# Kernel tuning notes

Measured on AMD Instinct MI355X. Metric: run time of the kernel, lower is better.

Reference implementation:

```python
import jax, jax.numpy as jnp
import numpy as np
from jax import lax

DIM = 1152
HEADS = 16
HEAD_DIM = 72  # HEADS*HEAD_DIM == DIM
HID = 4608     # int(DIM*4.0)
B = 2
N = 4096
EPS_RMS = 1e-6
EPS_LA = 1e-15


def setup_inputs() -> dict:
    key = jax.random.key(0)
    ks = jax.random.split(key, 12)
    w = lambda k, shape: (jax.random.normal(k, shape, jnp.float32) * 0.02)
    z = lambda n: jnp.zeros((n,), jnp.float32)
    return {
        "hidden_states": jax.random.normal(ks[0], (B, N, DIM), jnp.float32),
        "temb": jax.random.normal(ks[1], (B, 6 * DIM), jnp.float32),
        "scale_shift_table": jax.random.normal(ks[2], (6, DIM), jnp.float32) / np.float32(np.sqrt(DIM)),
        "Wq": w(ks[3], (DIM, DIM)), "bq": z(DIM),
        "Wk": w(ks[4], (DIM, DIM)), "bk": z(DIM),
        "Wv": w(ks[5], (DIM, DIM)), "bv": z(DIM),
        "Wo": w(ks[6], (DIM, DIM)), "bo": z(DIM),
        "W_inv": w(ks[7], (2 * HID, DIM)), "b_inv": z(2 * HID),   # 1x1 conv dim -> 2*hid
        "W_dw": w(ks[8], (2 * HID, 3)), "b_dw": z(2 * HID),       # depthwise k=3
        "W_pt": w(ks[9], (DIM, HID)),                              # 1x1 conv hid -> dim, no bias
    }


def _rms(x):
    # RMSNorm, elementwise_affine=False, eps=1e-6
    return x * lax.rsqrt(jnp.mean(x * x, axis=-1, keepdims=True) + EPS_RMS)


def reference(hidden_states, temb, scale_shift_table, Wq, bq, Wk, bk, Wv, bv, Wo, bo,
              W_inv, b_inv, W_dw, b_dw, W_pt):
    Bn, Nn, D = hidden_states.shape
    # adaLN-single modulation
    mods = scale_shift_table[None] + temb.reshape(Bn, 6, D)  # (B,6,D)
    shift_msa, scale_msa, gate_msa, shift_mlp, scale_mlp, gate_mlp = (
        mods[:, i][:, None, :] for i in range(6))  # each (B,1,D)

    x = _rms(hidden_states) * (1.0 + scale_msa) + shift_msa

    # --- Lite linear attention (ReLU kernel, denominator via padded-ones value) ---
    q = jax.nn.relu(x @ Wq.T + bq).reshape(Bn, Nn, HEADS, HEAD_DIM).transpose(0, 2, 1, 3)  # bhnd
    k = jax.nn.relu(x @ Wk.T + bk).reshape(Bn, Nn, HEADS, HEAD_DIM).transpose(0, 2, 1, 3)
    v = (x @ Wv.T + bv).reshape(Bn, Nn, HEADS, HEAD_DIM).transpose(0, 2, 1, 3)
    v = jnp.pad(v, ((0, 0), (0, 0), (0, 0), (0, 1)), constant_values=1.0)  # (B,h,N,d+1)
    kv = jnp.einsum('bhnd,bhne->bhde', k, v)        # (B,h,d,d+1)
    out = jnp.einsum('bhnd,bhde->bhne', q, kv)      # (B,h,N,d+1)
    out = out[..., :-1] / (out[..., -1:] + EPS_LA)  # numerator / denominator
    out = out.transpose(0, 2, 1, 3).reshape(Bn, Nn, D)
    attn_out = out @ Wo.T + bo

    hidden_states = gate_msa * attn_out + hidden_states

    # --- GLUMBConv FFN ---
    y = _rms(hidden_states) * (1.0 + scale_mlp) + shift_mlp
    y = jax.nn.silu(y @ W_inv.T + b_inv)            # inverted 1x1 conv + SiLU, (B,N,2*HID)
    yc = y.transpose(0, 2, 1)                        # (B,2*HID,N)
    yc = lax.conv_general_dilated(
        yc, W_dw[:, None, :], window_strides=(1,), padding=[(1, 1)],
        feature_group_count=2 * HID,
        dimension_numbers=('NCH', 'OIH', 'NCH')) + b_dw[None, :, None]
    xg, gate = jnp.split(yc, 2, axis=1)
    y = (xg * jax.nn.silu(gate)).transpose(0, 2, 1)  # (B,N,HID)
    ff = y @ W_pt.T                                   # point conv, no bias

    return hidden_states + gate_mlp * ff
```

## Files before the change

kernel.cpp:

```cpp
#include <hip/hip_runtime.h>
#include <hip/hip_bf16.h>

typedef __hip_bfloat16 bf16;
typedef short short8 __attribute__((ext_vector_type(8)));
typedef short short4v __attribute__((ext_vector_type(4)));
typedef float floatx4 __attribute__((ext_vector_type(4)));
typedef int int4v __attribute__((ext_vector_type(4)));

#define DIMC 1152
#define NTOK 8192
#define NSEQ 4096
#define HD 72
#define HDP 73
#define HIDC 4608
#define HID2 9216
#define QKVN 3456
#define KVH (HD * HDP)
#define PZ ((size_t)2048 * DIMC)
#define PZB ((size_t)4096 * DIMC)

#define DP 96
#define KVNT 128
#define KV_NITER 2
#define KV_CHUNKS 16

__device__ __forceinline__ float b2f(bf16 x) { return __bfloat162float(x); }
__device__ __forceinline__ bf16 f2b(float x) { return __float2bfloat16(x); }
__device__ __forceinline__ void st(float* p, float v) { *p = v; }
__device__ __forceinline__ void st(bf16* p, float v)  { *p = f2b(v); }
__device__ __forceinline__ float tf(float x) { return x; }
__device__ __forceinline__ float tf(bf16 x)  { return __bfloat162float(x); }
__device__ __forceinline__ float s2f(short s) {
    unsigned int u = ((unsigned int)(unsigned short)s) << 16;
    return __uint_as_float(u);
}
__device__ __forceinline__ short f2s(float f) {
    bf16 h = f2b(f);
    return *reinterpret_cast<short*>(&h);
}

__device__ __forceinline__ void gload_lds16(const bf16* g, short* l) {
    __builtin_amdgcn_global_load_lds(
        (const __attribute__((address_space(1))) void*)g,
        (__attribute__((address_space(3))) void*)l, 16, 0, 0);
}

__global__ void cvt_all_kernel(const float* __restrict__ s0, const float* __restrict__ s1,
                               const float* __restrict__ s2, const float* __restrict__ s3,
                               const float* __restrict__ s4, const float* __restrict__ s5,
                               bf16* __restrict__ dst) {
    int i = blockIdx.x * 256 + threadIdx.x;
    if (i >= 5308416) return;
    const float* src; int base;
    if (i < 1327104) {
        if (i < 331776)      { src = s0; base = 0; }
        else if (i < 663552) { src = s1; base = 331776; }
        else if (i < 995328) { src = s2; base = 663552; }
        else                 { src = s3; base = 995328; }
    } else if (i < 3981312)  { src = s4; base = 1327104; }
    else                     { src = s5; base = 3981312; }
    floatx4 v = ((const floatx4*)src)[i - base];
    bf16* o = dst + (size_t)i * 4;
    o[0] = f2b(v[0]); o[1] = f2b(v[1]); o[2] = f2b(v[2]); o[3] = f2b(v[3]);
}

__global__ void prep_kernel(const float* __restrict__ sst, const float* __restrict__ temb,
                            float* __restrict__ mods, const float* __restrict__ ba,
                            const float* __restrict__ bb, const float* __restrict__ bc,
                            float* __restrict__ bq) {
    int i = blockIdx.x * 256 + threadIdx.x;
    if (i < 2 * 6 * DIMC) {
        mods[i] = sst[i % (6 * DIMC)] + temb[i];
    } else if (i < 2 * 6 * DIMC + DIMC) {
        int j = i - 2 * 6 * DIMC;
        bq[j] = ba[j]; bq[j + DIMC] = bb[j]; bq[j + 2 * DIMC] = bc[j];
    }
}

template<typename T>
__global__ void rmsmod_kernel(const T* __restrict__ h, const float* __restrict__ mods,
                              int shift_idx, int scale_idx, bf16* __restrict__ xout) {
    int token = blockIdx.x;
    int b = token >> 12;
    int tid = threadIdx.x;
    int wave = tid >> 6, lane = tid & 63;
    const T* hp = h + (size_t)token * DIMC;

    float v[8];
    float s = 0.f;
    if (tid < 144) {
        if constexpr (sizeof(T) == 4) {
            floatx4 a = *(const floatx4*)((const float*)hp + tid * 8);
            floatx4 c = *(const floatx4*)((const float*)hp + tid * 8 + 4);
            v[0]=a[0]; v[1]=a[1]; v[2]=a[2]; v[3]=a[3];
            v[4]=c[0]; v[5]=c[1]; v[6]=c[2]; v[7]=c[3];
        } else {
            short8 a = *(const short8*)((const short*)hp + tid * 8);
            #pragma unroll
            for (int j = 0; j < 8; j++) v[j] = s2f(a[j]);
        }
        #pragma unroll
        for (int j = 0; j < 8; j++) s += v[j] * v[j];
    }
    #pragma unroll
    for (int off = 32; off > 0; off >>= 1) s += __shfl_down(s, off);
    __shared__ float wsum[4];
    if (lane == 0) wsum[wave] = s;
    __syncthreads();
    float tot = wsum[0] + wsum[1] + wsum[2] + wsum[3];
    float r = rsqrtf(tot / (float)DIMC + 1e-6f);

    if (tid < 144) {
        const float* sh = mods + (size_t)(b * 6 + shift_idx) * DIMC + tid * 8;
        const float* sc = mods + (size_t)(b * 6 + scale_idx) * DIMC + tid * 8;
        floatx4 sh0 = *(const floatx4*)sh, sh1 = *(const floatx4*)(sh + 4);
        floatx4 sc0 = *(const floatx4*)sc, sc1 = *(const floatx4*)(sc + 4);
        short8 o;
        o[0] = f2s(v[0] * r * (1.f + sc0[0]) + sh0[0]);
        o[1] = f2s(v[1] * r * (1.f + sc0[1]) + sh0[1]);
        o[2] = f2s(v[2] * r * (1.f + sc0[2]) + sh0[2]);
        o[3] = f2s(v[3] * r * (1.f + sc0[3]) + sh0[3]);
        o[4] = f2s(v[4] * r * (1.f + sc1[0]) + sh1[0]);
        o[5] = f2s(v[5] * r * (1.f + sc1[1]) + sh1[1]);
        o[6] = f2s(v[6] * r * (1.f + sc1[2]) + sh1[2]);
        o[7] = f2s(v[7] * r * (1.f + sc1[3]) + sh1[3]);
        *(short8*)((short*)xout + (size_t)token * DIMC + tid * 8) = o;
    }
}

template<int MODE, typename OT>
__global__ __launch_bounds__(256, 2)
void gemm_kernel(const bf16* __restrict__ A, const bf16* __restrict__ W,
                 const float* __restrict__ bias, const float* __restrict__ mods,
                 int gate_idx, int m_off, const float* __restrict__ resid,
                 OT* __restrict__ out, int N, int Kfull, int Klen,
                 size_t zstride, int bm_lo, int bm_hi) {
    const int bm = blockIdx.x;
    if (bm < bm_lo || bm >= bm_hi) return;
    const int koff = blockIdx.z * Klen;
    __shared__ __align__(16) short As[128 * 64];
    __shared__ __align__(16) short Bs[128 * 64];
    const int tid = threadIdx.x;
    const int wave = tid >> 6;
    const int lane = tid & 63;
    const int quad = lane >> 4;
    const int l16 = lane & 15;
    const int wm = (wave & 1) * 64;
    const int wn = (wave >> 1) * 64;
    const int bn = blockIdx.y;

    floatx4 acc[4][4];
    #pragma unroll
    for (int i = 0; i < 4; i++)
        #pragma unroll
        for (int j = 0; j < 4; j++)
            #pragma unroll
            for (int r = 0; r < 4; r++) acc[i][j][r] = 0.0f;

    const int lrow8 = lane >> 3;
    const int scol = ((lane & 7) ^ lrow8) * 8;
    const bf16* gA = A + (size_t)(bm * 128 + wave * 8 + lrow8) * Kfull + koff + scol;
    const bf16* gB = W + (size_t)(bn * 128 + wave * 8 + lrow8) * Kfull + koff + scol;
    short* lA = &As[wave * 512];
    short* lB = &Bs[wave * 512];
    const size_t rstep = (size_t)32 * Kfull;

    for (int k0 = 0; k0 < Klen; k0 += 64) {
        __syncthreads();
        #pragma unroll
        for (int j = 0; j < 4; j++) gload_lds16(gA + j * rstep + k0, lA + j * 2048);
        #pragma unroll
        for (int j = 0; j < 4; j++) gload_lds16(gB + j * rstep + k0, lB + j * 2048);
        __syncthreads();
        short8 af[2][4], bfr[2][4];
        #pragma unroll
        for (int i = 0; i < 4; i++) {
            const int ra = wm + i * 16 + l16;
            const int rb = wn + i * 16 + l16;
            #pragma unroll
            for (int kk = 0; kk < 2; kk++) {
                af[kk][i]  = *(const short8*)&As[ra * 64 + (((kk * 4 + quad) ^ (ra & 7)) * 8)];
                bfr[kk][i] = *(const short8*)&Bs[rb * 64 + (((kk * 4 + quad) ^ (rb & 7)) * 8)];
            }
        }
        #pragma unroll
        for (int kk = 0; kk < 2; kk++)
            #pragma unroll
            for (int i = 0; i < 4; i++)
                #pragma unroll
                for (int j = 0; j < 4; j++)
                    acc[i][j] = __builtin_amdgcn_mfma_f32_16x16x32_bf16(af[kk][i], bfr[kk][j], acc[i][j], 0, 0, 0);
    }

    #pragma unroll
    for (int i = 0; i < 4; i++) {
        #pragma unroll
        for (int j = 0; j < 4; j++) {
            const int col = bn * 128 + wn + j * 16 + l16;
            #pragma unroll
            for (int r = 0; r < 4; r++) {
                const int m = bm * 128 + wm + i * 16 + quad * 4 + r;
                float v = acc[i][j][r];
                float o;
                if (MODE == 0) {
                    o = v + bias[col];
                    if (col < 2 * DIMC) o = fmaxf(o, 0.f);
                } else if (MODE == 2) {
                    int b = (m + m_off) >> 12;
                    o = mods[(size_t)(b * 6 + gate_idx) * DIMC + col] * (v + bias[col])
                        + resid[(size_t)m * DIMC + col];
                } else if (MODE == 3) {
                    float sv = v + bias[col];
                    o = sv / (1.f + __expf(-sv));
                } else if (MODE == 6) {
                    const bf16* tr = (const bf16*)resid;
                    int b = m >> 12;
                    o = tf(tr[(size_t)m * DIMC + col])
                        + mods[(size_t)(b * 6 + gate_idx) * DIMC + col] * v;
                } else {
                    o = v;
                }
                st(&out[zstride * blockIdx.z + (size_t)m * N + col], o);
            }
        }
    }
}

template<int NP>
__global__ void reduce_kernel(const float* __restrict__ part, const bf16* __restrict__ trunk,
                              const float* __restrict__ mods, int b, int r0, size_t pstride,
                              float* __restrict__ out) {
    int i4 = (blockIdx.x * 256 + threadIdx.x) * 4;
    int col = i4 % DIMC;
    floatx4 s = *(const floatx4*)(part + i4);
    #pragma unroll
    for (int p = 1; p < NP; ++p) {
        floatx4 t = *(const floatx4*)(part + (size_t)p * pstride + i4);
        s[0] += t[0]; s[1] += t[1]; s[2] += t[2]; s[3] += t[3];
    }
    size_t gidx = ((size_t)b * NSEQ + r0) * DIMC + i4;
    short4v tr = *(const short4v*)((const short*)trunk + gidx);
    floatx4 g = *(const floatx4*)(mods + (size_t)(b * 6 + 5) * DIMC + col);
    floatx4 o;
    #pragma unroll
    for (int j = 0; j < 4; ++j) o[j] = s2f(tr[j]) + g[j] * s[j];
    *(floatx4*)(out + gidx) = o;
}

__device__ __forceinline__ int kvaddr(int row, int n) {
    return row * KVNT + ((((n >> 3) ^ (row & 7))) << 3) + (n & 7);
}

__global__ __launch_bounds__(256, 3)
void attn_kv_kernel(const bf16* __restrict__ qkv, float* __restrict__ part) {
    const int chunk = blockIdx.x;
    const int h = blockIdx.y;
    const int b = blockIdx.z;
    __shared__ __align__(16) short kl[DP * KVNT];
    __shared__ __align__(16) short vl[DP * KVNT];
    const int tid = threadIdx.x;
    const int wave = tid >> 6, lane = tid & 63;
    const int quad = lane >> 4, l16 = lane & 15;
    const int wd = (wave & 1) * 48;
    const int we = (wave >> 1) * 48;

    for (int i = tid; i < 24 * KVNT; i += 256) {
        kl[72 * KVNT + i] = 0;
        vl[72 * KVNT + i] = (i < KVNT) ? (short)0x3F80 : (short)0;
    }

    floatx4 acc[3][3];
    #pragma unroll
    for (int i = 0; i < 3; i++)
        #pragma unroll
        for (int j = 0; j < 3; j++)
            #pragma unroll
            for (int r = 0; r < 4; r++) acc[i][j][r] = 0.0f;

    const size_t tok0 = (size_t)b * NSEQ + (size_t)chunk * (KVNT * KV_NITER);
    for (int it = 0; it < KV_NITER; ++it) {
        __syncthreads();
        const short* rb = (const short*)qkv + (tok0 + (size_t)it * KVNT) * QKVN + h * HD;
        #pragma unroll
        for (int p = 0; p < 5; ++p) {
            int idx = p * 256 + tid;
            int o = idx >> 7, n = idx & 127;
            if (o < 9) {
                const short* g = rb + (size_t)n * QKVN + o * 8;
                short8 kk = *(const short8*)(g + DIMC);
                short8 vv = *(const short8*)(g + 2 * DIMC);
                #pragma unroll
                for (int j = 0; j < 8; ++j) {
                    kl[kvaddr(o * 8 + j, n)] = kk[j];
                    vl[kvaddr(o * 8 + j, n)] = vv[j];
                }
            }
        }
        __syncthreads();
        #pragma unroll
        for (int ks = 0; ks < 4; ++ks) {
            const int nb = ks * 32 + quad * 8;
            short8 af[3], bfv[3];
            #pragma unroll
            for (int i = 0; i < 3; ++i) {
                const int ra = wd + i * 16 + l16;
                const int rbn = we + i * 16 + l16;
                af[i]  = *(const short8*)&kl[ra * KVNT + ((((nb >> 3) ^ (ra & 7))) << 3)];
                bfv[i] = *(const short8*)&vl[rbn * KVNT + ((((nb >> 3) ^ (rbn & 7))) << 3)];
            }
            #pragma unroll
            for (int i = 0; i < 3; ++i)
                #pragma unroll
                for (int j = 0; j < 3; ++j)
                    acc[i][j] = __builtin_amdgcn_mfma_f32_16x16x32_bf16(af[i], bfv[j], acc[i][j], 0, 0, 0);
        }
    }

    float* op = part + ((size_t)((b * 16 + h) * KV_CHUNKS + chunk)) * KVH;
    #pragma unroll
    for (int i = 0; i < 3; ++i) {
        const int dbase = wd + i * 16 + quad * 4;
        #pragma unroll
        for (int j = 0; j < 3; ++j) {
            const int e = we + j * 16 + l16;
            if (e < HDP) {
                #pragma unroll
                for (int r = 0; r < 4; ++r) {
                    const int d = dbase + r;
                    if (d < HD) op[d * HDP + e] = acc[i][j][r];
                }
            }
        }
    }
}

__global__ void kvred_kernel(const float* __restrict__ part, float* __restrict__ kvout) {
    int i = blockIdx.x * 256 + threadIdx.x;
    if (i >= 32 * KVH) return;
    int bh = i / KVH, cell = i - bh * KVH;
    const float* p = part + ((size_t)bh * KV_CHUNKS) * KVH + cell;
    float s = 0.f;
    #pragma unroll
    for (int c = 0; c < KV_CHUNKS; ++c) s += p[(size_t)c * KVH];
    kvout[i] = s;
}

__global__ __launch_bounds__(256, 2)
void attn_out_kernel(const bf16* __restrict__ qkv, const float* __restrict__ kv,
                     bf16* __restrict__ outa) {
    const int chunk = blockIdx.x;
    const int h = blockIdx.y;
    const int b = blockIdx.z;
    __shared__ __align__(16) short ql[128 * 128];
    __shared__ __align__(16) short kvt[80 * 128];
    const int tid = threadIdx.x;
    const int wave = tid >> 6, lane = tid & 63;
    const int quad = lane >> 4, l16 = lane & 15;
    const int wm = wave * 32;

    const short* qbase = (const short*)qkv + ((size_t)(b * NSEQ) + (size_t)chunk * 128) * QKVN + h * HD;
    #pragma unroll
    for (int t = 0; t < 8; ++t) {
        int idx = t * 256 + tid;
        int o = idx >> 7, n = idx & 127;
        short8 vv = {0, 0, 0, 0, 0, 0, 0, 0};
        if (o < 9) vv = *(const short8*)(qbase + (size_t)n * QKVN + o * 8);
        *(short8*)&ql[n * 128 + ((o ^ (n & 7)) << 3)] = vv;
    }
    const float* kp = kv + (size_t)(b * 16 + h) * KVH;
    #pragma unroll
    for (int t = 0; t < 5; ++t) {
        int idx = t * 256 + tid;
        int o = idx / 80, e = idx - (idx / 80) * 80;
        short8 vv = {0, 0, 0, 0, 0, 0, 0, 0};
        if (e < HDP && o < 9) {
            #pragma unroll
            for (int j = 0; j < 8; ++j) {
                int d = o * 8 + j;
                if (d < HD) vv[j] = f2s(kp[(size_t)d * HDP + e]);
            }
        }
        *(short8*)&kvt[e * 128 + ((o ^ (e & 7)) << 3)] = vv;
    }
    __syncthreads();

    floatx4 acc[2][5];
    #pragma unroll
    for (int i = 0; i < 2; ++i)
        #pragma unroll
        for (int j = 0; j < 5; ++j)
            #pragma unroll
            for (int r = 0; r < 4; ++r) acc[i][j][r] = 0.0f;

    #pragma unroll
    for (int kk = 0; kk < 3; ++kk) {
        const int s = kk * 4 + quad;
        short8 af[2];
        #pragma unroll
        for (int i = 0; i < 2; ++i) {
            const int ra = wm + i * 16 + l16;
            af[i] = *(const short8*)&ql[ra * 128 + ((s ^ (ra & 7)) << 3)];
        }
        #pragma unroll
        for (int j = 0; j < 5; ++j) {
            const int rb = j * 16 + l16;
            short8 bfv = *(const short8*)&kvt[rb * 128 + ((s ^ (rb & 7)) << 3)];
            #pragma unroll
            for (int i = 0; i < 2; ++i)
                acc[i][j] = __builtin_amdgcn_mfma_f32_16x16x32_bf16(af[i], bfv, acc[i][j], 0, 0, 0);
        }
    }

    #pragma unroll
    for (int i = 0; i < 2; ++i) {
        #pragma unroll
        for (int r = 0; r < 4; ++r) {
            float den = __shfl(acc[i][4][r], (lane & 48) | 8);
            float inv = 1.0f / (den + 1e-15f);
            const int m = wm + i * 16 + quad * 4 + r;
            bf16* op = outa + ((size_t)(b * NSEQ) + (size_t)chunk * 128 + m) * DIMC + h * HD;
            #pragma unroll
            for (int j = 0; j < 5; ++j) {
                const int e = j * 16 + l16;
                if (e < HD) op[e] = f2b(acc[i][j][r] * inv);
            }
        }
    }
}

__global__ __launch_bounds__(576)
void dwglu_kernel(const bf16* __restrict__ ybuf, const float* __restrict__ wdw,
                  const float* __restrict__ bdw, int r0, int rowoff, bf16* __restrict__ outg) {
    int bid = blockIdx.x;
    int nper = gridDim.x >> 3;
    int nl = (bid & 7) * nper + (bid >> 3);
    int g = (r0 + nl) & (NSEQ - 1);
    int c = threadIdx.x * 8;
    int cg = c + HIDC;
    size_t base = (size_t)(nl + rowoff) * HID2;
    const short* yb = (const short*)ybuf;
    short8 zr = {0, 0, 0, 0, 0, 0, 0, 0};
    bool hm = (g > 0), hp = (g < NSEQ - 1);
    short8 xm = hm ? *(const short8*)(yb + base - HID2 + c)  : zr;
    short8 x0 =      *(const short8*)(yb + base + c);
    short8 xp = hp ? *(const short8*)(yb + base + HID2 + c)  : zr;
    short8 gm = hm ? *(const short8*)(yb + base - HID2 + cg) : zr;
    short8 g0 =      *(const short8*)(yb + base + cg);
    short8 gp = hp ? *(const short8*)(yb + base + HID2 + cg) : zr;
    float wx[24], wg[24], bxv[8], bgv[8];
    #pragma unroll
    for (int t = 0; t < 6; t++) {
        *(floatx4*)&wx[t * 4] = *(const floatx4*)(wdw + (size_t)c * 3 + t * 4);
        *(floatx4*)&wg[t * 4] = *(const floatx4*)(wdw + (size_t)cg * 3 + t * 4);
    }
    *(floatx4*)&bxv[0] = *(const floatx4*)(bdw + c);
    *(floatx4*)&bxv[4] = *(const floatx4*)(bdw + c + 4);
    *(floatx4*)&bgv[0] = *(const floatx4*)(bdw + cg);
    *(floatx4*)&bgv[4] = *(const floatx4*)(bdw + cg + 4);
    short8 o;
    #pragma unroll
    for (int j = 0; j < 8; j++) {
        float a  = s2f(xm[j]) * wx[j * 3] + s2f(x0[j]) * wx[j * 3 + 1]
                 + s2f(xp[j]) * wx[j * 3 + 2] + bxv[j];
        float gg = s2f(gm[j]) * wg[j * 3] + s2f(g0[j]) * wg[j * 3 + 1]
                 + s2f(gp[j]) * wg[j * 3 + 2] + bgv[j];
        float sg = gg / (1.f + __expf(-gg));
        o[j] = f2s(a * sg);
    }
    *(short8*)((short*)outg + (size_t)nl * HIDC + c) = o;
}

extern "C" void kernel_launch(void* const* d_in, const int* in_sizes, int n_in,
                              void* d_out, int out_size, void* d_ws, size_t ws_size,
                              hipStream_t stream) {
    const float* h_in = (const float*)d_in[0];
    const float* temb = (const float*)d_in[1];
    const float* sst  = (const float*)d_in[2];
    const float* Wq = (const float*)d_in[3];   const float* bq_ = (const float*)d_in[4];
    const float* Wk = (const float*)d_in[5];   const float* bk_ = (const float*)d_in[6];
    const float* Wv = (const float*)d_in[7];   const float* bv_ = (const float*)d_in[8];
    const float* Wo = (const float*)d_in[9];   const float* bo_ = (const float*)d_in[10];
    const float* Winv = (const float*)d_in[11]; const float* binv = (const float*)d_in[12];
    const float* Wdw  = (const float*)d_in[13]; const float* bdw  = (const float*)d_in[14];
    const float* Wpt  = (const float*)d_in[15];
    float* out = (float*)d_out;

    const int WSMALL = DIMC * DIMC;
    const int WINVN  = HID2 * DIMC;
    const int WPTN   = DIMC * HIDC;

    char* basep = (char*)d_ws;
    size_t off = 0;
    auto alloc = [&](size_t bytes) -> char* {
        char* p = basep + off;
        off += (bytes + 255) & ~(size_t)255;
        return p;
    };
    float* modsb = (float*)alloc((size_t)2 * 6 * DIMC * 4);
    float* kvb   = (float*)alloc((size_t)32 * KVH * 4);
    float* kvpart = (float*)alloc((size_t)32 * KV_CHUNKS * KVH * 4);
    float* bqkv  = (float*)alloc((size_t)QKVN * 4);
    bf16* wqkv = (bf16*)alloc((size_t)3 * WSMALL * 2);
    bf16* wob  = (bf16*)alloc((size_t)WSMALL * 2);
    bf16* wib  = (bf16*)alloc((size_t)WINVN * 2);
    bf16* wpb  = (bf16*)alloc((size_t)WPTN * 2);
    bf16* bx    = (bf16*)alloc((size_t)NTOK * DIMC * 2);
    bf16* trunk = (bf16*)alloc((size_t)NTOK * DIMC * 2);

    const size_t BGLU2 = (size_t)NTOK * HIDC * 2;
    const size_t BBIG2 = (size_t)NTOK * HID2 * 2;
    const size_t BGLU_B = (size_t)NSEQ * HIDC * 2;
    const size_t BBIG_B = (size_t)NSEQ * HID2 * 2;
    int tier = (ws_size >= off + BGLU2 + BBIG2 + 1024) ? 0
             : (ws_size >= off + BGLU_B + BBIG_B + 1024) ? 1 : 2;
    char* R = alloc(tier == 0 ? (BGLU2 + BBIG2)
                  : tier == 1 ? (BGLU_B + BBIG_B) : (size_t)61341696);
    bf16* qkvb = (bf16*)R;

    cvt_all_kernel<<<20736, 256, 0, stream>>>(Wq, Wk, Wv, Wo, Winv, Wpt, wqkv);
    prep_kernel<<<59, 256, 0, stream>>>(sst, temb, modsb, bq_, bk_, bv_, bqkv);
    rmsmod_kernel<float><<<NTOK, 256, 0, stream>>>(h_in, modsb, 0, 1, bx);

    gemm_kernel<0, bf16><<<dim3(NTOK / 128, QKVN / 128), 256, 0, stream>>>(
        bx, wqkv, bqkv, nullptr, 0, 0, nullptr, qkvb, QKVN, DIMC, DIMC, 0, 0, 1 << 30);

    attn_kv_kernel<<<dim3(KV_CHUNKS, 16, 2), 256, 0, stream>>>(qkvb, kvpart);
    kvred_kernel<<<(32 * KVH + 255) / 256, 256, 0, stream>>>(kvpart, kvb);
    attn_out_kernel<<<dim3(32, 16, 2), 256, 0, stream>>>(qkvb, kvb, bx);
    gemm_kernel<2, bf16><<<dim3(NTOK / 128, DIMC / 128), 256, 0, stream>>>(
        bx, wob, bo_, modsb, 2, 0, h_in, trunk, DIMC, DIMC, DIMC, 0, 0, 1 << 30);
    rmsmod_kernel<bf16><<<NTOK, 256, 0, stream>>>(trunk, modsb, 3, 4, bx);

    if (tier == 0) {
        bf16* bglu = (bf16*)R;
        bf16* bbig = (bf16*)(R + BGLU2);
        gemm_kernel<3, bf16><<<dim3(NTOK / 128, HID2 / 128), 256, 0, stream>>>(
            bx, wib, binv, nullptr, 0, 0, nullptr, bbig, HID2, DIMC, DIMC, 0, 0, 1 << 30);
        dwglu_kernel<<<dim3(NTOK), 576, 0, stream>>>(bbig, Wdw, bdw, 0, 0, bglu);
        gemm_kernel<6, float><<<dim3(NTOK / 128, DIMC / 128), 256, 0, stream>>>(
            bglu, wpb, nullptr, modsb, 5, 0, (const float*)trunk, out, DIMC, HIDC, HIDC,
            0, 0, 1 << 30);
    } else if (tier == 1) {
        bf16*  bglu = (bf16*)R;
        bf16*  bbig = (bf16*)(R + BGLU_B);
        float* partials = (float*)(R + BGLU_B);
        for (int b = 0; b < 2; ++b) {
            const bf16* Ainv = bx + (size_t)b * NSEQ * DIMC;
            gemm_kernel<3, bf16><<<dim3(NSEQ / 128, HID2 / 128), 256, 0, stream>>>(
                Ainv, wib, binv, nullptr, 0, 0, nullptr, bbig, HID2, DIMC, DIMC, 0, 0, 1 << 30);
            dwglu_kernel<<<dim3(NSEQ), 576, 0, stream>>>(bbig, Wdw, bdw, 0, 0, bglu);
            gemm_kernel<5, float><<<dim3(32, DIMC / 128, 2), 256, 0, stream>>>(
                bglu, wpb, nullptr, nullptr, 0, 0, nullptr, partials, DIMC, HIDC, HIDC / 2,
                PZB, 0, 1 << 30);
            reduce_kernel<2><<<(int)(PZB / 1024), 256, 0, stream>>>(partials, trunk, modsb, b, 0,
                                                                    PZB, out);
        }
    } else {
        bf16*  bglu_c   = (bf16*)R;
        bf16*  bbig_c   = (bf16*)(R + (size_t)18874368);
        float* partials = (float*)(R + (size_t)18874368);
        for (int b = 0; b < 2; ++b) {
            for (int c = 0; c < 2; ++c) {
                int r0 = c * 2048;
                int lo = (c == 0) ? 1 : 0;
                int hi = (c == 0) ? 18 : 17;
                const bf16* Ainv = bx + ((size_t)(b * NSEQ + r0)) * DIMC - (size_t)128 * DIMC;
                gemm_kernel<3, bf16><<<dim3(18, HID2 / 128), 256, 0, stream>>>(
                    Ainv, wib, binv, nullptr, 0, 0, nullptr, bbig_c, HID2, DIMC, DIMC, 0, lo, hi);
                dwglu_kernel<<<dim3(2048), 576, 0, stream>>>(bbig_c, Wdw, bdw, r0, 128, bglu_c);
                gemm_kernel<5, float><<<dim3(16, DIMC / 128, 4), 256, 0, stream>>>(
                    bglu_c, wpb, nullptr, nullptr, 0, 0, nullptr, partials, DIMC, HIDC, HIDC / 4,
                    PZ, 0, 1 << 30);
                reduce_kernel<4><<<(int)(PZ / 1024), 256, 0, stream>>>(partials, trunk, modsb, b,
                                                                       r0, PZ, out);
            }
        }
    }
}
```

Baseline: 798.3 us.

## Alias workspace buffers so the single-pass FFN path fits in less memory

Reworks the workspace layout so the tier-0 FFN path needs only one batch-sized expanded buffer instead of two. The QKV, normalized-activation, KV-partial and small weight buffers now live inside the reused region, where their lifetimes end before the FFN buffers are written. The inverted-conv GEMM and depthwise GLU now run per batch, but the final point-conv GEMM still runs once with its fused epilogue. This lets a smaller workspace take the path without split-K partials and the extra reduce kernel, at the cost of tight buffer aliasing that depends on launch ordering.

```diff
diff --git a/kernel.cpp b/kernel.cpp
--- a/kernel.cpp
+++ b/kernel.cpp
@@ -48,19 +48,23 @@
 __global__ void cvt_all_kernel(const float* __restrict__ s0, const float* __restrict__ s1,
                                const float* __restrict__ s2, const float* __restrict__ s3,
                                const float* __restrict__ s4, const float* __restrict__ s5,
-                               bf16* __restrict__ dst) {
+                               bf16* __restrict__ dstA, bf16* __restrict__ dstB) {
     int i = blockIdx.x * 256 + threadIdx.x;
     if (i >= 5308416) return;
-    const float* src; int base;
+    const float* src; int base, ib; bf16* dst;
     if (i < 1327104) {
+        dst = dstA; ib = i;
         if (i < 331776)      { src = s0; base = 0; }
         else if (i < 663552) { src = s1; base = 331776; }
         else if (i < 995328) { src = s2; base = 663552; }
         else                 { src = s3; base = 995328; }
-    } else if (i < 3981312)  { src = s4; base = 1327104; }
-    else                     { src = s5; base = 3981312; }
+    } else {
+        dst = dstB; ib = i - 1327104;
+        if (i < 3981312)     { src = s4; base = 1327104; }
+        else                 { src = s5; base = 3981312; }
+    }
     floatx4 v = ((const floatx4*)src)[i - base];
-    bf16* o = dst + (size_t)i * 4;
+    bf16* o = dst + (size_t)ib * 4;
     o[0] = f2b(v[0]); o[1] = f2b(v[1]); o[2] = f2b(v[2]); o[3] = f2b(v[3]);
 }
 
@@ -498,26 +502,45 @@
     };
     float* modsb = (float*)alloc((size_t)2 * 6 * DIMC * 4);
     float* kvb   = (float*)alloc((size_t)32 * KVH * 4);
-    float* kvpart = (float*)alloc((size_t)32 * KV_CHUNKS * KVH * 4);
     float* bqkv  = (float*)alloc((size_t)QKVN * 4);
-    bf16* wqkv = (bf16*)alloc((size_t)3 * WSMALL * 2);
-    bf16* wob  = (bf16*)alloc((size_t)WSMALL * 2);
     bf16* wib  = (bf16*)alloc((size_t)WINVN * 2);
     bf16* wpb  = (bf16*)alloc((size_t)WPTN * 2);
-    bf16* bx    = (bf16*)alloc((size_t)NTOK * DIMC * 2);
     bf16* trunk = (bf16*)alloc((size_t)NTOK * DIMC * 2);
 
-    const size_t BGLU2 = (size_t)NTOK * HIDC * 2;
-    const size_t BBIG2 = (size_t)NTOK * HID2 * 2;
-    const size_t BGLU_B = (size_t)NSEQ * HIDC * 2;
-    const size_t BBIG_B = (size_t)NSEQ * HID2 * 2;
-    int tier = (ws_size >= off + BGLU2 + BBIG2 + 1024) ? 0
-             : (ws_size >= off + BGLU_B + BBIG_B + 1024) ? 1 : 2;
-    char* R = alloc(tier == 0 ? (BGLU2 + BBIG2)
-                  : tier == 1 ? (BGLU_B + BBIG_B) : (size_t)61341696);
-    bf16* qkvb = (bf16*)R;
-
-    cvt_all_kernel<<<20736, 256, 0, stream>>>(Wq, Wk, Wv, Wo, Winv, Wpt, wqkv);
+    const size_t QKVB_B  = (size_t)NTOK * QKVN * 2;
+    const size_t BX_B    = (size_t)NTOK * DIMC * 2;
+    const size_t BGLU2   = (size_t)NTOK * HIDC * 2;
+    const size_t BBIG_B  = (size_t)NSEQ * HID2 * 2;
+    const size_t KVPART_B = (size_t)32 * KV_CHUNKS * KVH * 4;
+    const size_t WQKV_B  = (size_t)3 * WSMALL * 2;
+    const size_t WOB_B   = (size_t)WSMALL * 2;
+    const size_t BGLU_B  = (size_t)NSEQ * HIDC * 2;
+
+    bool tier0 = (ws_size >= off + BGLU2 + BBIG_B + 1024);
+
+    bf16 *qkvb, *bx, *wqkv, *wob;
+    float* kvpart;
+    char* R;
+    if (tier0) {
+        R = alloc(BGLU2 + BBIG_B);
+        qkvb   = (bf16*)R;
+        bx     = (bf16*)(R + QKVB_B);
+        kvpart = (float*)(R + BGLU2);
+        wqkv   = (bf16*)(R + BGLU2 + KVPART_B);
+        wob    = (bf16*)(R + BGLU2 + KVPART_B + WQKV_B);
+    } else {
+        kvpart = (float*)alloc(KVPART_B);
+        wqkv   = (bf16*)alloc(WQKV_B);
+        wob    = (bf16*)alloc(WOB_B);
+        bx     = (bf16*)alloc(BX_B);
+        bool tier1 = (ws_size >= off + BGLU_B + BBIG_B + 1024);
+        R = alloc(tier1 ? (BGLU_B + BBIG_B) : (size_t)61341696);
+        qkvb = (bf16*)R;
+        if (!tier1) {  }
+    }
+    bool tier1 = !tier0 && (ws_size >= ((size_t)(((char*)bx - basep)) + BX_B + 255 + BGLU_B + BBIG_B + 1024));
+
+    cvt_all_kernel<<<20736, 256, 0, stream>>>(Wq, Wk, Wv, Wo, Winv, Wpt, wqkv, wib);
     prep_kernel<<<59, 256, 0, stream>>>(sst, temb, modsb, bq_, bk_, bv_, bqkv);
     rmsmod_kernel<float><<<NTOK, 256, 0, stream>>>(h_in, modsb, 0, 1, bx);
 
@@ -531,16 +554,20 @@
         bx, wob, bo_, modsb, 2, 0, h_in, trunk, DIMC, DIMC, DIMC, 0, 0, 1 << 30);
     rmsmod_kernel<bf16><<<NTOK, 256, 0, stream>>>(trunk, modsb, 3, 4, bx);
 
-    if (tier == 0) {
+    if (tier0) {
         bf16* bglu = (bf16*)R;
         bf16* bbig = (bf16*)(R + BGLU2);
-        gemm_kernel<3, bf16><<<dim3(NTOK / 128, HID2 / 128), 256, 0, stream>>>(
-            bx, wib, binv, nullptr, 0, 0, nullptr, bbig, HID2, DIMC, DIMC, 0, 0, 1 << 30);
-        dwglu_kernel<<<dim3(NTOK), 576, 0, stream>>>(bbig, Wdw, bdw, 0, 0, bglu);
+        for (int b = 0; b < 2; ++b) {
+            const bf16* Ainv = bx + (size_t)b * NSEQ * DIMC;
+            gemm_kernel<3, bf16><<<dim3(NSEQ / 128, HID2 / 128), 256, 0, stream>>>(
+                Ainv, wib, binv, nullptr, 0, 0, nullptr, bbig, HID2, DIMC, DIMC, 0, 0, 1 << 30);
+            dwglu_kernel<<<dim3(NSEQ), 576, 0, stream>>>(
+                bbig, Wdw, bdw, 0, 0, bglu + (size_t)b * NSEQ * HIDC);
+        }
         gemm_kernel<6, float><<<dim3(NTOK / 128, DIMC / 128), 256, 0, stream>>>(
             bglu, wpb, nullptr, modsb, 5, 0, (const float*)trunk, out, DIMC, HIDC, HIDC,
             0, 0, 1 << 30);
-    } else if (tier == 1) {
+    } else if (tier1) {
         bf16*  bglu = (bf16*)R;
         bf16*  bbig = (bf16*)(R + BGLU_B);
         float* partials = (float*)(R + BGLU_B);
```

Result: faster. 756.4 us (-5.3%).
